# Optimization experiments

Measured on AMD Instinct MI355X. Metric: run time of the kernel, lower is better.

## Reference

```python
import jax, jax.numpy as jnp
import numpy as np

HIDDEN = 64
INPUT_DIM = 128
DEMO_DIM = 12
ATT_WIDTH = 1e7  # history_only=True, attention_width=None -> causal


def setup_inputs() -> dict:
    key = jax.random.key(0)
    ks = jax.random.split(key, 8)
    B, T = 4, 512
    inp = {
        "input": jax.random.normal(ks[0], (B, T, INPUT_DIM), dtype=jnp.float32),
        "demo": jax.random.normal(ks[1], (B, DEMO_DIM), dtype=jnp.float32),
        "Wt": jax.random.normal(ks[2], (INPUT_DIM, HIDDEN), dtype=jnp.float32) * 0.08,
        "Wx": jax.random.normal(ks[3], (INPUT_DIM, HIDDEN), dtype=jnp.float32) * 0.08,
        "Wd": jax.random.normal(ks[4], (DEMO_DIM, HIDDEN), dtype=jnp.float32) * 0.25,
        "bh": jnp.zeros((HIDDEN,), dtype=jnp.float32),
        "Wa": jax.random.normal(ks[5], (HIDDEN, 1), dtype=jnp.float32) * 0.12,
        "ba": jnp.zeros((1,), dtype=jnp.float32),
    }
    return inp


def reference(input, demo, Wt, Wx, Wd, bh, Wa, ba):
    B, T, D = input.shape
    # additive attention scores via broadcasted [B,T,T,H] intermediate
    q = (input @ Wt)[:, :, None, :]          # [B,T,1,H]
    k = (input @ Wx)[:, None, :, :]          # [B,1,T,H]
    d = (demo @ Wd)[:, None, None, :]        # [B,1,1,H]
    h = jnp.tanh(q + k + d + bh)             # [B,T,T,H]
    e = (h @ Wa)[..., 0] + ba[0]             # [B,T,T]
    # custom softmax: exp(e - rowmax) BEFORE masking, then mask, then normalize
    e = jnp.exp(e - jnp.max(e, axis=-1, keepdims=True))
    idx = jnp.arange(T, dtype=jnp.float32)
    lower = idx[:, None] - (ATT_WIDTH - 1.0)  # history_only
    upper = lower + ATT_WIDTH
    mask = ((lower <= idx[None, :]) & (idx[None, :] < upper)).astype(e.dtype)
    e = e * mask
    s = jnp.sum(e, axis=-1, keepdims=True)
    e = e / (s + 1e-7)
    v = jnp.einsum('bts,bsd->btd', e, input)  # [B,T,D]
    return (v, e)
```

## Files before the change

### kernel.cpp

```cpp
#include <hip/hip_runtime.h>
#include <math.h>

#define B_ 4
#define T_ 512
#define D_ 128
#define H_ 64
#define DEMO_ 12
#define LOG2E 1.4426950408889634f
#define SC2   (2.0f * LOG2E)

typedef float float4v __attribute__((ext_vector_type(4)));
typedef float float2v __attribute__((ext_vector_type(2)));

__global__ __launch_bounds__(256) void prep_kernel(
    const float* __restrict__ input, const float* __restrict__ demo,
    const float* __restrict__ Wt, const float* __restrict__ Wx,
    const float* __restrict__ Wd, const float* __restrict__ bh,
    const float* __restrict__ Wa, const float* __restrict__ ba,
    float* __restrict__ Q, float* __restrict__ K2T, float* __restrict__ Cs)
{
    __shared__ float in_sh[8 * D_];
    int tid  = threadIdx.x;
    int row0 = blockIdx.x * 8;
    int b    = row0 >> 9;

    #pragma unroll
    for (int k = 0; k < 4; ++k)
        in_sh[tid + 256 * k] = input[row0 * D_ + tid + 256 * k];
    __syncthreads();

    int h  = tid & 63;
    int rr = tid >> 6;

    float dB = bh[h];
    #pragma unroll
    for (int kk = 0; kk < DEMO_; ++kk)
        dB = fmaf(demo[b * DEMO_ + kk], Wd[kk * H_ + h], dB);

    float q0 = 0.f, q1 = 0.f, x0 = 0.f, x1 = 0.f;
    #pragma unroll 8
    for (int k = 0; k < D_; ++k) {
        float wt = Wt[k * H_ + h];
        float wx = Wx[k * H_ + h];
        float a0 = in_sh[rr * D_ + k];
        float a1 = in_sh[(rr + 4) * D_ + k];
        q0 = fmaf(a0, wt, q0);
        q1 = fmaf(a1, wt, q1);
        x0 = fmaf(a0, wx, x0);
        x1 = fmaf(a1, wx, x1);
    }

    int ra = row0 + rr, rb = row0 + rr + 4;
    Q[ra * H_ + h] = q0 * SC2;
    Q[rb * H_ + h] = q1 * SC2;
    int ta = ra & (T_ - 1), tb = rb & (T_ - 1);
    K2T[(b * H_ + h) * T_ + ta] = (x0 + dB) * SC2;
    K2T[(b * H_ + h) * T_ + tb] = (x1 + dB) * SC2;

    if (blockIdx.x == 0 && tid < 64) {
        float w = Wa[tid];
        #pragma unroll
        for (int off = 32; off; off >>= 1) w += __shfl_down(w, off, 64);
        if (tid == 0) Cs[0] = (ba[0] + w) * LOG2E;
    }
}

__global__ __launch_bounds__(512, 4) void attn_kernel(
    const float* __restrict__ input,
    const float* __restrict__ Qs, const float* __restrict__ K2T,
    const float* __restrict__ Wa, const float* __restrict__ Cs,
    float* __restrict__ out_v, float* __restrict__ out_e)
{
    __shared__ float   qsh[H_ * 4];
    __shared__ float   p_sh[T_ * 4];
    __shared__ float4v red_m[8];
    __shared__ float4v red_s[8];
    __shared__ float   partial[16][4 * D_];

    int tid  = threadIdx.x;
    int y    = blockIdx.x;
    int b    = blockIdx.y;
    int lane = tid & 63, wv = tid >> 6;
    int j    = tid;
    int iA0  = 2 * y,       iA1 = iA0 + 1;
    int iB0  = 510 - 2 * y, iB1 = iB0 + 1;

    if (tid < 256) {
        int h  = tid >> 2, r = tid & 3;
        int ir = (r < 2) ? (iA0 + r) : (iB0 + r - 2);
        qsh[tid] = Qs[(size_t)(b * T_ + ir) * H_ + h];
    }
    __syncthreads();

    const float* k2p = K2T + (size_t)b * H_ * T_ + j;
    float CL   = Cs[0];
    bool  actA = (wv << 6) <= iA1;
    bool  actB = (wv << 6) <= iB1;

    float aA0 = 0.f, aA1 = 0.f, aB0 = 0.f, aB1 = 0.f;
    if (actA) {
        #pragma unroll 2
        for (int h0 = 0; h0 < H_; h0 += 8) {
            float kv[8];
            #pragma unroll
            for (int u = 0; u < 8; ++u) kv[u] = k2p[(size_t)(h0 + u) * T_];
            #pragma unroll
            for (int u = 0; u < 8; ++u) {
                float wa   = Wa[h0 + u];
                float4v q4 = *(const float4v*)&qsh[(h0 + u) * 4];
                float e0 = __builtin_amdgcn_exp2f(q4[0] + kv[u]);
                float e1 = __builtin_amdgcn_exp2f(q4[1] + kv[u]);
                float e2 = __builtin_amdgcn_exp2f(q4[2] + kv[u]);
                float e3 = __builtin_amdgcn_exp2f(q4[3] + kv[u]);
                aA0 = fmaf(wa, __builtin_amdgcn_rcpf(1.0f + e0), aA0);
                aA1 = fmaf(wa, __builtin_amdgcn_rcpf(1.0f + e1), aA1);
                aB0 = fmaf(wa, __builtin_amdgcn_rcpf(1.0f + e2), aB0);
                aB1 = fmaf(wa, __builtin_amdgcn_rcpf(1.0f + e3), aB1);
            }
        }
    } else if (actB) {
        #pragma unroll 2
        for (int h0 = 0; h0 < H_; h0 += 8) {
            float kv[8];
            #pragma unroll
            for (int u = 0; u < 8; ++u) kv[u] = k2p[(size_t)(h0 + u) * T_];
            #pragma unroll
            for (int u = 0; u < 8; ++u) {
                float wa   = Wa[h0 + u];
                float2v q2 = *(const float2v*)&qsh[(h0 + u) * 4 + 2];
                float e2 = __builtin_amdgcn_exp2f(q2[0] + kv[u]);
                float e3 = __builtin_amdgcn_exp2f(q2[1] + kv[u]);
                aB0 = fmaf(wa, __builtin_amdgcn_rcpf(1.0f + e2), aB0);
                aB1 = fmaf(wa, __builtin_amdgcn_rcpf(1.0f + e3), aB1);
            }
        }
    }

    float eg0 = (j <= iA0) ? fmaf(-SC2, aA0, CL) : -INFINITY;
    float eg1 = (j <= iA1) ? fmaf(-SC2, aA1, CL) : -INFINITY;
    float eg2 = (j <= iB0) ? fmaf(-SC2, aB0, CL) : -INFINITY;
    float eg3 = (j <= iB1) ? fmaf(-SC2, aB1, CL) : -INFINITY;

    float M0 = eg0, M1 = eg1, M2 = eg2, M3 = eg3;
    #pragma unroll
    for (int off = 32; off; off >>= 1) {
        M0 = fmaxf(M0, __shfl_down(M0, off, 64));
        M1 = fmaxf(M1, __shfl_down(M1, off, 64));
        M2 = fmaxf(M2, __shfl_down(M2, off, 64));
        M3 = fmaxf(M3, __shfl_down(M3, off, 64));
    }
    if (lane == 0) red_m[wv] = (float4v){M0, M1, M2, M3};
    __syncthreads();
    {
        float4v m = red_m[0];
        #pragma unroll
        for (int w = 1; w < 8; ++w) {
            float4v mw = red_m[w];
            m[0] = fmaxf(m[0], mw[0]); m[1] = fmaxf(m[1], mw[1]);
            m[2] = fmaxf(m[2], mw[2]); m[3] = fmaxf(m[3], mw[3]);
        }
        M0 = m[0]; M1 = m[1]; M2 = m[2]; M3 = m[3];
    }

    float p0 = (j <= iA0) ? __builtin_amdgcn_exp2f(eg0 - M0) : 0.0f;
    float p1 = (j <= iA1) ? __builtin_amdgcn_exp2f(eg1 - M1) : 0.0f;
    float p2 = (j <= iB0) ? __builtin_amdgcn_exp2f(eg2 - M2) : 0.0f;
    float p3 = (j <= iB1) ? __builtin_amdgcn_exp2f(eg3 - M3) : 0.0f;
    *(float4v*)&p_sh[j * 4] = (float4v){p0, p1, p2, p3};

    float S0 = p0, S1 = p1, S2 = p2, S3 = p3;
    #pragma unroll
    for (int off = 32; off; off >>= 1) {
        S0 += __shfl_down(S0, off, 64);
        S1 += __shfl_down(S1, off, 64);
        S2 += __shfl_down(S2, off, 64);
        S3 += __shfl_down(S3, off, 64);
    }
    if (lane == 0) red_s[wv] = (float4v){S0, S1, S2, S3};
    __syncthreads();

    float inv0, inv1, inv2, inv3;
    {
        float4v s = red_s[0];
        #pragma unroll
        for (int w = 1; w < 8; ++w) {
            float4v sw = red_s[w];
            s[0] += sw[0]; s[1] += sw[1]; s[2] += sw[2]; s[3] += sw[3];
        }
        inv0 = __builtin_amdgcn_rcpf(s[0] + 1e-7f);
        inv1 = __builtin_amdgcn_rcpf(s[1] + 1e-7f);
        inv2 = __builtin_amdgcn_rcpf(s[2] + 1e-7f);
        inv3 = __builtin_amdgcn_rcpf(s[3] + 1e-7f);
    }

    {
        int s  = tid >> 5, d4 = tid & 31;
        float4v va0 = {0,0,0,0}, va1 = {0,0,0,0}, va2 = {0,0,0,0}, va3 = {0,0,0,0};
        if ((s << 5) <= iB1) {
            const float* inp = input + ((size_t)(b * T_) + (s << 5)) * D_ + (d4 << 2);
            const float* pp  = p_sh + (s << 5) * 4;
            #pragma unroll 4
            for (int jj = 0; jj < 32; ++jj) {
                float4v x  = *(const float4v*)(inp + (size_t)jj * D_);
                float4v p4 = *(const float4v*)(pp + jj * 4);
                va0 += x * p4[0];
                va1 += x * p4[1];
                va2 += x * p4[2];
                va3 += x * p4[3];
            }
        }
        *(float4v*)&partial[s][0 * D_ + (d4 << 2)] = va0;
        *(float4v*)&partial[s][1 * D_ + (d4 << 2)] = va1;
        *(float4v*)&partial[s][2 * D_ + (d4 << 2)] = va2;
        *(float4v*)&partial[s][3 * D_ + (d4 << 2)] = va3;
    }
    __syncthreads();

    {
        int r  = tid >> 7, d = tid & 127;
        float v = 0.f;
        #pragma unroll
        for (int ss = 0; ss < 16; ++ss) v += partial[ss][r * D_ + d];
        int   ir  = (r < 2) ? (iA0 + r) : (iB0 + r - 2);
        float inv = (r == 0) ? inv0 : (r == 1) ? inv1 : (r == 2) ? inv2 : inv3;
        out_v[(size_t)(b * T_ + ir) * D_ + d] = v * inv;
    }

    out_e[((size_t)(b * T_ + iA0)) * T_ + j] = p0 * inv0;
    out_e[((size_t)(b * T_ + iA1)) * T_ + j] = p1 * inv1;
    out_e[((size_t)(b * T_ + iB0)) * T_ + j] = p2 * inv2;
    out_e[((size_t)(b * T_ + iB1)) * T_ + j] = p3 * inv3;
}

extern "C" void kernel_launch(void* const* d_in, const int* in_sizes, int n_in,
                              void* d_out, int out_size, void* d_ws, size_t ws_size,
                              hipStream_t stream)
{
    const float* input = (const float*)d_in[0];
    const float* demo  = (const float*)d_in[1];
    const float* Wt    = (const float*)d_in[2];
    const float* Wx    = (const float*)d_in[3];
    const float* Wd    = (const float*)d_in[4];
    const float* bh    = (const float*)d_in[5];
    const float* Wa    = (const float*)d_in[6];
    const float* ba    = (const float*)d_in[7];

    float* out_v = (float*)d_out;
    float* out_e = out_v + (size_t)B_ * T_ * D_;

    float* Q   = (float*)d_ws;
    float* K2T = Q + (size_t)B_ * T_ * H_;
    float* Cs  = K2T + (size_t)B_ * H_ * T_;

    prep_kernel<<<dim3(B_ * T_ / 8), 256, 0, stream>>>(input, demo, Wt, Wx, Wd, bh,
                                                       Wa, ba, Q, K2T, Cs);
    attn_kernel<<<dim3(128, B_), 512, 0, stream>>>(input, Q, K2T, Wa, Cs, out_v, out_e);
}
```

Baseline: 93.08 us.

## Drop softmax max pass, prefetch K in attention, split-K the prep kernel

The attention kernel no longer computes the row max before exponentiating. The additive scores are bounded because tanh is bounded, so exp2 is applied directly and normalisation cancels the shift. This removes four shuffle reductions, a shared-memory round trip and a barrier. The score loop now double-buffers the K2T loads one chunk ahead to hide global latency. The prep kernel moves to 4-row blocks of 512 threads with a split-K reduction through shared memory and a vectorised K2T store, which doubles the grid size. Skipping the max relies on the scores staying small enough that exp2 cannot overflow, and that depends on the magnitude of Wa.

```diff
diff --git a/kernel.cpp b/kernel.cpp
--- a/kernel.cpp
+++ b/kernel.cpp
@@ -12,50 +12,61 @@
 typedef float float4v __attribute__((ext_vector_type(4)));
 typedef float float2v __attribute__((ext_vector_type(2)));
 
-__global__ __launch_bounds__(256) void prep_kernel(
+__global__ __launch_bounds__(512) void prep_kernel(
     const float* __restrict__ input, const float* __restrict__ demo,
     const float* __restrict__ Wt, const float* __restrict__ Wx,
     const float* __restrict__ Wd, const float* __restrict__ bh,
     const float* __restrict__ Wa, const float* __restrict__ ba,
     float* __restrict__ Q, float* __restrict__ K2T, float* __restrict__ Cs)
 {
-    __shared__ float in_sh[8 * D_];
+    __shared__ float in_sh[4 * D_];
+    __shared__ float acc_sh[2][4][2][H_];
+    __shared__ float k2_sh[4][H_];
+
     int tid  = threadIdx.x;
-    int row0 = blockIdx.x * 8;
+    int row0 = blockIdx.x * 4;
     int b    = row0 >> 9;
 
-    #pragma unroll
-    for (int k = 0; k < 4; ++k)
-        in_sh[tid + 256 * k] = input[row0 * D_ + tid + 256 * k];
-    __syncthreads();
-
-    int h  = tid & 63;
-    int rr = tid >> 6;
-
-    float dB = bh[h];
-    #pragma unroll
-    for (int kk = 0; kk < DEMO_; ++kk)
-        dB = fmaf(demo[b * DEMO_ + kk], Wd[kk * H_ + h], dB);
-
-    float q0 = 0.f, q1 = 0.f, x0 = 0.f, x1 = 0.f;
+    in_sh[tid] = input[(size_t)row0 * D_ + tid];
+    __syncthreads();
+
+    int h    = tid & 63;
+    int s    = tid >> 6;
+    int r    = s & 3;
+    int half = s >> 2;
+
+    const float* ish = &in_sh[r * D_ + half * 64];
+    const float* wt  = Wt + (size_t)(half * 64) * H_ + h;
+    const float* wx  = Wx + (size_t)(half * 64) * H_ + h;
+    float q = 0.f, x = 0.f;
     #pragma unroll 8
-    for (int k = 0; k < D_; ++k) {
-        float wt = Wt[k * H_ + h];
-        float wx = Wx[k * H_ + h];
-        float a0 = in_sh[rr * D_ + k];
-        float a1 = in_sh[(rr + 4) * D_ + k];
-        q0 = fmaf(a0, wt, q0);
-        q1 = fmaf(a1, wt, q1);
-        x0 = fmaf(a0, wx, x0);
-        x1 = fmaf(a1, wx, x1);
-    }
-
-    int ra = row0 + rr, rb = row0 + rr + 4;
-    Q[ra * H_ + h] = q0 * SC2;
-    Q[rb * H_ + h] = q1 * SC2;
-    int ta = ra & (T_ - 1), tb = rb & (T_ - 1);
-    K2T[(b * H_ + h) * T_ + ta] = (x0 + dB) * SC2;
-    K2T[(b * H_ + h) * T_ + tb] = (x1 + dB) * SC2;
+    for (int k = 0; k < 64; ++k) {
+        float a = ish[k];
+        q = fmaf(a, wt[(size_t)k * H_], q);
+        x = fmaf(a, wx[(size_t)k * H_], x);
+    }
+    acc_sh[half][r][0][h] = q;
+    acc_sh[half][r][1][h] = x;
+    __syncthreads();
+
+    if (tid < 256) {
+        int h2 = tid & 63, r2 = tid >> 6;
+        float dB = bh[h2];
+        #pragma unroll
+        for (int k = 0; k < DEMO_; ++k)
+            dB = fmaf(demo[b * DEMO_ + k], Wd[k * H_ + h2], dB);
+        float qv = (acc_sh[0][r2][0][h2] + acc_sh[1][r2][0][h2]) * SC2;
+        float xv = (acc_sh[0][r2][1][h2] + acc_sh[1][r2][1][h2] + dB) * SC2;
+        Q[(size_t)(row0 + r2) * H_ + h2] = qv;
+        k2_sh[r2][h2] = xv;
+    }
+    __syncthreads();
+
+    if (tid < 64) {
+        float4v v = { k2_sh[0][tid], k2_sh[1][tid], k2_sh[2][tid], k2_sh[3][tid] };
+        int t0 = row0 & (T_ - 1);
+        *(float4v*)&K2T[((size_t)(b * H_ + tid)) * T_ + t0] = v;
+    }
 
     if (blockIdx.x == 0 && tid < 64) {
         float w = Wa[tid];
@@ -73,7 +84,6 @@
 {
     __shared__ float   qsh[H_ * 4];
     __shared__ float   p_sh[T_ * 4];
-    __shared__ float4v red_m[8];
     __shared__ float4v red_s[8];
     __shared__ float   partial[16][4 * D_];
 
@@ -99,73 +109,63 @@
 
     float aA0 = 0.f, aA1 = 0.f, aB0 = 0.f, aB1 = 0.f;
     if (actA) {
-        #pragma unroll 2
+        float kc[8], kn[8];
+        #pragma unroll
+        for (int u = 0; u < 8; ++u) kc[u] = k2p[(size_t)u * T_];
+        #pragma unroll 1
         for (int h0 = 0; h0 < H_; h0 += 8) {
-            float kv[8];
-            #pragma unroll
-            for (int u = 0; u < 8; ++u) kv[u] = k2p[(size_t)(h0 + u) * T_];
+            if (h0 + 8 < H_) {
+                #pragma unroll
+                for (int u = 0; u < 8; ++u) kn[u] = k2p[(size_t)(h0 + 8 + u) * T_];
+            }
             #pragma unroll
             for (int u = 0; u < 8; ++u) {
                 float wa   = Wa[h0 + u];
                 float4v q4 = *(const float4v*)&qsh[(h0 + u) * 4];
-                float e0 = __builtin_amdgcn_exp2f(q4[0] + kv[u]);
-                float e1 = __builtin_amdgcn_exp2f(q4[1] + kv[u]);
-                float e2 = __builtin_amdgcn_exp2f(q4[2] + kv[u]);
-                float e3 = __builtin_amdgcn_exp2f(q4[3] + kv[u]);
+                float e0 = __builtin_amdgcn_exp2f(q4[0] + kc[u]);
+                float e1 = __builtin_amdgcn_exp2f(q4[1] + kc[u]);
+                float e2 = __builtin_amdgcn_exp2f(q4[2] + kc[u]);
+                float e3 = __builtin_amdgcn_exp2f(q4[3] + kc[u]);
                 aA0 = fmaf(wa, __builtin_amdgcn_rcpf(1.0f + e0), aA0);
                 aA1 = fmaf(wa, __builtin_amdgcn_rcpf(1.0f + e1), aA1);
                 aB0 = fmaf(wa, __builtin_amdgcn_rcpf(1.0f + e2), aB0);
                 aB1 = fmaf(wa, __builtin_amdgcn_rcpf(1.0f + e3), aB1);
             }
+            if (h0 + 8 < H_) {
+                #pragma unroll
+                for (int u = 0; u < 8; ++u) kc[u] = kn[u];
+            }
         }
     } else if (actB) {
-        #pragma unroll 2
+        float kc[8], kn[8];
+        #pragma unroll
+        for (int u = 0; u < 8; ++u) kc[u] = k2p[(size_t)u * T_];
+        #pragma unroll 1
         for (int h0 = 0; h0 < H_; h0 += 8) {
-            float kv[8];
-            #pragma unroll
-            for (int u = 0; u < 8; ++u) kv[u] = k2p[(size_t)(h0 + u) * T_];
+            if (h0 + 8 < H_) {
+                #pragma unroll
+                for (int u = 0; u < 8; ++u) kn[u] = k2p[(size_t)(h0 + 8 + u) * T_];
+            }
             #pragma unroll
             for (int u = 0; u < 8; ++u) {
                 float wa   = Wa[h0 + u];
                 float2v q2 = *(const float2v*)&qsh[(h0 + u) * 4 + 2];
-                float e2 = __builtin_amdgcn_exp2f(q2[0] + kv[u]);
-                float e3 = __builtin_amdgcn_exp2f(q2[1] + kv[u]);
+                float e2 = __builtin_amdgcn_exp2f(q2[0] + kc[u]);
+                float e3 = __builtin_amdgcn_exp2f(q2[1] + kc[u]);
                 aB0 = fmaf(wa, __builtin_amdgcn_rcpf(1.0f + e2), aB0);
                 aB1 = fmaf(wa, __builtin_amdgcn_rcpf(1.0f + e3), aB1);
             }
-        }
-    }
-
-    float eg0 = (j <= iA0) ? fmaf(-SC2, aA0, CL) : -INFINITY;
-    float eg1 = (j <= iA1) ? fmaf(-SC2, aA1, CL) : -INFINITY;
-    float eg2 = (j <= iB0) ? fmaf(-SC2, aB0, CL) : -INFINITY;
-    float eg3 = (j <= iB1) ? fmaf(-SC2, aB1, CL) : -INFINITY;
-
-    float M0 = eg0, M1 = eg1, M2 = eg2, M3 = eg3;
-    #pragma unroll
-    for (int off = 32; off; off >>= 1) {
-        M0 = fmaxf(M0, __shfl_down(M0, off, 64));
-        M1 = fmaxf(M1, __shfl_down(M1, off, 64));
-        M2 = fmaxf(M2, __shfl_down(M2, off, 64));
-        M3 = fmaxf(M3, __shfl_down(M3, off, 64));
-    }
-    if (lane == 0) red_m[wv] = (float4v){M0, M1, M2, M3};
-    __syncthreads();
-    {
-        float4v m = red_m[0];
-        #pragma unroll
-        for (int w = 1; w < 8; ++w) {
-            float4v mw = red_m[w];
-            m[0] = fmaxf(m[0], mw[0]); m[1] = fmaxf(m[1], mw[1]);
-            m[2] = fmaxf(m[2], mw[2]); m[3] = fmaxf(m[3], mw[3]);
-        }
-        M0 = m[0]; M1 = m[1]; M2 = m[2]; M3 = m[3];
-    }
-
-    float p0 = (j <= iA0) ? __builtin_amdgcn_exp2f(eg0 - M0) : 0.0f;
-    float p1 = (j <= iA1) ? __builtin_amdgcn_exp2f(eg1 - M1) : 0.0f;
-    float p2 = (j <= iB0) ? __builtin_amdgcn_exp2f(eg2 - M2) : 0.0f;
-    float p3 = (j <= iB1) ? __builtin_amdgcn_exp2f(eg3 - M3) : 0.0f;
+            if (h0 + 8 < H_) {
+                #pragma unroll
+                for (int u = 0; u < 8; ++u) kc[u] = kn[u];
+            }
+        }
+    }
+
+    float p0 = (j <= iA0) ? __builtin_amdgcn_exp2f(fmaf(-SC2, aA0, CL)) : 0.0f;
+    float p1 = (j <= iA1) ? __builtin_amdgcn_exp2f(fmaf(-SC2, aA1, CL)) : 0.0f;
+    float p2 = (j <= iB0) ? __builtin_amdgcn_exp2f(fmaf(-SC2, aB0, CL)) : 0.0f;
+    float p3 = (j <= iB1) ? __builtin_amdgcn_exp2f(fmaf(-SC2, aB1, CL)) : 0.0f;
     *(float4v*)&p_sh[j * 4] = (float4v){p0, p1, p2, p3};
 
     float S0 = p0, S1 = p1, S2 = p2, S3 = p3;
@@ -252,7 +252,7 @@
     float* K2T = Q + (size_t)B_ * T_ * H_;
     float* Cs  = K2T + (size_t)B_ * H_ * T_;
 
-    prep_kernel<<<dim3(B_ * T_ / 8), 256, 0, stream>>>(input, demo, Wt, Wx, Wd, bh,
+    prep_kernel<<<dim3(B_ * T_ / 4), 512, 0, stream>>>(input, demo, Wt, Wx, Wd, bh,
                                                        Wa, ba, Q, K2T, Cs);
     attn_kernel<<<dim3(128, B_), 512, 0, stream>>>(input, Q, K2T, Wa, Cs, out_v, out_e);
 }
```

Result: no change. 91.54 us (-1.7%).
